# Kernel optimization log

Hardware: AMD Instinct MI355X
Metric: run time of the kernel (lower is better)

The kernel has to match this reference:

```python
import jax, jax.numpy as jnp
import numpy as np

N, H, V = 4096, 1024, 16384


def setup_inputs() -> dict:
    key = jax.random.key(0)
    k1, k2, k3, k4 = jax.random.split(key, 4)
    _input = jax.random.normal(k1, (N, H), dtype=jnp.float32)
    weight = jax.random.normal(k2, (V, H), dtype=jnp.float32) * (1.0 / np.sqrt(H))
    target = jax.random.normal(k3, (N, V), dtype=jnp.float32)
    bias = jax.random.normal(k4, (V,), dtype=jnp.float32)
    return {"_input": _input, "weight": weight, "target": target, "bias": bias}


def reference(_input, weight, target, bias):
    # Fused linear + MSE with reduction='mean':
    # logits = _input @ weight.T + bias  -> (N, V)
    # loss = mean((logits - target)**2) over all N*V elements
    logits = jnp.einsum("nh,vh->nv", _input, weight) + bias
    diff = logits - target
    return jnp.mean(diff * diff)
```

## Files before the change

### kernel.cpp

```cpp
#include <hip/hip_runtime.h>
#include <hip/hip_bf16.h>
#include <stdint.h>

#define N_ 4096
#define H_ 1024
#define V_ 16384

using i32x8  = __attribute__((ext_vector_type(8))) int;
using f32x16 = __attribute__((ext_vector_type(16))) float;

__global__ void cast2_f32_to_fp8(const float* __restrict__ in0, uint8_t* __restrict__ out0,
                                 const float* __restrict__ in1, uint8_t* __restrict__ out1,
                                 int nblk0) {
    const float* in;
    uint8_t* out;
    int bid;
    if (blockIdx.x < (unsigned)nblk0) { in = in0; out = out0; bid = blockIdx.x; }
    else                              { in = in1; out = out1; bid = blockIdx.x - nblk0; }
    size_t i = ((size_t)bid * blockDim.x + threadIdx.x) * 8;
    float4 a = *(const float4*)(in + i);
    float4 b = *(const float4*)(in + i + 4);
    int lo = __builtin_amdgcn_cvt_pk_fp8_f32(a.x, a.y, 0, 0);
    lo     = __builtin_amdgcn_cvt_pk_fp8_f32(a.z, a.w, lo, 1);
    int hi = __builtin_amdgcn_cvt_pk_fp8_f32(b.x, b.y, 0, 0);
    hi     = __builtin_amdgcn_cvt_pk_fp8_f32(b.z, b.w, hi, 1);
    *(int2*)(out + i) = make_int2(lo, hi);
}

#define BM 128
#define BN 128
#define BK 128

__global__ __launch_bounds__(256, 2) void gemm_mse(
    const uint8_t* __restrict__ A8,
    const uint8_t* __restrict__ W8,
    const float*  __restrict__ target,
    const float*  __restrict__ bias,
    float* __restrict__ partials)
{
    __shared__ uint8_t As[2 * 8 * 1024];
    __shared__ uint8_t Bs[2 * 8 * 1024];
    __shared__ float red[4];

    const int tid  = threadIdx.x;
    const int w    = tid >> 6;
    const int lane = tid & 63;
    const int l32  = lane & 31;
    const int half = lane >> 5;
    const int wm   = w >> 1;
    const int wn   = w & 1;

    const int flat = blockIdx.x;
    const int xcd  = flat & 7;
    const int idx  = flat >> 3;
    const int tx   = xcd * 16 + (idx & 15);
    const int ty   = idx >> 4;

    const int rowBase = ty * BM;
    const int colBase = tx * BN;

    f32x16 acc[2][2];
#pragma unroll
    for (int i = 0; i < 2; ++i)
#pragma unroll
        for (int j = 0; j < 2; ++j)
#pragma unroll
            for (int r = 0; r < 16; ++r) acc[i][j][r] = 0.f;

    const int ldrow = lane >> 2;
    const int ldkq  = (lane & 3) ^ ((ldrow + (ldrow >> 2)) & 3);

    const int rl  = lane & 15;
    const int rcb = (lane >> 4) & 1;
    const int fl  = (rl + (rl >> 2)) & 3;
    const uint8_t* aPtr[2][2];
    const uint8_t* bPtr[2][2];
#pragma unroll
    for (int i = 0; i < 2; ++i)
#pragma unroll
        for (int c = 0; c < 2; ++c) {
            const int slot = rl * 4 + (((half << 1) + c) ^ fl);
            aPtr[i][c] = As + (size_t)((wm * 2 + i) * 2 + rcb) * 1024 + slot * 16;
            bPtr[i][c] = Bs + (size_t)((wn * 2 + i) * 2 + rcb) * 1024 + slot * 16;
        }

    for (int k0 = 0; k0 < H_; k0 += BK) {
        __syncthreads();
#pragma unroll
        for (int h = 0; h < 2; ++h) {
#pragma unroll
            for (int c = 0; c < 2; ++c) {
                const int chunkid = w * 2 + c;
                const int kOff = k0 + h * 64 + ldkq * 16;
                const uint8_t* ga = A8 + (size_t)(rowBase + chunkid * 16 + ldrow) * H_ + kOff;
                __builtin_amdgcn_global_load_lds(
                    (const __attribute__((address_space(1))) void*)ga,
                    (__attribute__((address_space(3))) void*)(As + h * 8192 + chunkid * 1024), 16, 0, 0);
                const uint8_t* gb = W8 + (size_t)(colBase + chunkid * 16 + ldrow) * H_ + kOff;
                __builtin_amdgcn_global_load_lds(
                    (const __attribute__((address_space(1))) void*)gb,
                    (__attribute__((address_space(3))) void*)(Bs + h * 8192 + chunkid * 1024), 16, 0, 0);
            }
        }
        __syncthreads();

#pragma unroll
        for (int h = 0; h < 2; ++h) {
            i32x8 af[2], bq[2];
#pragma unroll
            for (int i = 0; i < 2; ++i) {
                int4 a0 = *(const int4*)(aPtr[i][0] + h * 8192);
                int4 a1 = *(const int4*)(aPtr[i][1] + h * 8192);
                af[i][0] = a0.x; af[i][1] = a0.y; af[i][2] = a0.z; af[i][3] = a0.w;
                af[i][4] = a1.x; af[i][5] = a1.y; af[i][6] = a1.z; af[i][7] = a1.w;
                int4 b0 = *(const int4*)(bPtr[i][0] + h * 8192);
                int4 b1 = *(const int4*)(bPtr[i][1] + h * 8192);
                bq[i][0] = b0.x; bq[i][1] = b0.y; bq[i][2] = b0.z; bq[i][3] = b0.w;
                bq[i][4] = b1.x; bq[i][5] = b1.y; bq[i][6] = b1.z; bq[i][7] = b1.w;
            }
#pragma unroll
            for (int i = 0; i < 2; ++i)
#pragma unroll
                for (int j = 0; j < 2; ++j)
                    acc[i][j] = __builtin_amdgcn_mfma_scale_f32_32x32x64_f8f6f4(
                        af[i], bq[j], acc[i][j],
                        0 , 0 ,
                        0, 0x7F7F7F7F,
                        0, 0x7F7F7F7F);
        }
    }

    float sum = 0.f;
    float biasj[2];
#pragma unroll
    for (int j = 0; j < 2; ++j) biasj[j] = bias[colBase + wn * 64 + j * 32 + l32];

#pragma unroll
    for (int i = 0; i < 2; ++i) {
#pragma unroll
        for (int r = 0; r < 16; ++r) {
            const int row = (r & 3) + 8 * (r >> 2) + 4 * half;
            const int gm = rowBase + wm * 64 + i * 32 + row;
            const float* trow = target + (size_t)gm * V_ + colBase + wn * 64 + l32;
#pragma unroll
            for (int j = 0; j < 2; ++j) {
                float d = acc[i][j][r] + biasj[j] - trow[j * 32];
                sum += d * d;
            }
        }
    }

#pragma unroll
    for (int off = 32; off; off >>= 1) sum += __shfl_down(sum, off, 64);
    if (lane == 0) red[w] = sum;
    __syncthreads();
    if (tid == 0)
        partials[flat] = red[0] + red[1] + red[2] + red[3];
}

__global__ void finalize_kernel(const float* __restrict__ partials, float* __restrict__ out, int n) {
    float s = 0.f;
    for (int i = threadIdx.x; i < n; i += 256) s += partials[i];
#pragma unroll
    for (int off = 32; off; off >>= 1) s += __shfl_down(s, off, 64);
    __shared__ float red[4];
    const int w = threadIdx.x >> 6, lane = threadIdx.x & 63;
    if (lane == 0) red[w] = s;
    __syncthreads();
    if (threadIdx.x == 0)
        out[0] = (red[0] + red[1] + red[2] + red[3]) * (1.0f / ((float)N_ * (float)V_));
}

extern "C" void kernel_launch(void* const* d_in, const int* in_sizes, int n_in,
                              void* d_out, int out_size, void* d_ws, size_t ws_size,
                              hipStream_t stream) {
    const float* input  = (const float*)d_in[0];
    const float* weight = (const float*)d_in[1];
    const float* target = (const float*)d_in[2];
    const float* bias   = (const float*)d_in[3];
    float* out = (float*)d_out;

    uint8_t* A8 = (uint8_t*)d_ws;
    uint8_t* W8 = A8 + (size_t)N_ * H_;
    float* partials = (float*)(W8 + (size_t)V_ * H_);

    const int nblk0 = (N_ * H_) / (256 * 8);
    const int nblk1 = (V_ * H_) / (256 * 8);
    cast2_f32_to_fp8<<<nblk0 + nblk1, 256, 0, stream>>>(input, A8, weight, W8, nblk0);

    const int nblocks = (V_ / BN) * (N_ / BM);
    gemm_mse<<<nblocks, 256, 0, stream>>>(A8, W8, target, bias, partials);

    finalize_kernel<<<1, 256, 0, stream>>>(partials, out, nblocks);
}
```

Before: 452.2 us.

## Enlarge GEMM tile to 256x256 with double-buffered LDS prefetch pipeline

Doubles the block tile to 256x256 with 512 threads (8 waves, each computing 128x64) to raise operand reuse per LDS byte and halve global fp8 reloads. Adds a 128KB dynamic-LDS double buffer so the next K-slice is loaded with global_load_lds while MFMAs run on the current one, replacing the two per-iteration __syncthreads with a single waitcnt+barrier. Raises wave priority around the MFMA block. The large LDS footprint limits occupancy to one block per CU and increases register pressure from the doubled accumulators.

```diff
diff --git a/kernel.cpp b/kernel.cpp
--- a/kernel.cpp
+++ b/kernel.cpp
@@ -27,41 +27,42 @@
     *(int2*)(out + i) = make_int2(lo, hi);
 }
 
-#define BM 128
-#define BN 128
+#define BM 256
+#define BN 256
 #define BK 128
 
-__global__ __launch_bounds__(256, 2) void gemm_mse(
+__global__ __launch_bounds__(512, 2) void gemm_mse(
     const uint8_t* __restrict__ A8,
     const uint8_t* __restrict__ W8,
     const float*  __restrict__ target,
     const float*  __restrict__ bias,
     float* __restrict__ partials)
 {
-    __shared__ uint8_t As[2 * 8 * 1024];
-    __shared__ uint8_t Bs[2 * 8 * 1024];
-    __shared__ float red[4];
+    extern __shared__ __align__(16) uint8_t smem[];
+    uint8_t* As = smem;
+    uint8_t* Bs = smem + 65536;
+    __shared__ float red[8];
 
     const int tid  = threadIdx.x;
     const int w    = tid >> 6;
     const int lane = tid & 63;
     const int l32  = lane & 31;
     const int half = lane >> 5;
-    const int wm   = w >> 1;
-    const int wn   = w & 1;
+    const int wm   = w >> 2;
+    const int wn   = w & 3;
 
     const int flat = blockIdx.x;
     const int xcd  = flat & 7;
     const int idx  = flat >> 3;
-    const int tx   = xcd * 16 + (idx & 15);
-    const int ty   = idx >> 4;
+    const int tx   = xcd * 8 + (idx & 7);
+    const int ty   = idx >> 3;
 
     const int rowBase = ty * BM;
     const int colBase = tx * BN;
 
-    f32x16 acc[2][2];
-#pragma unroll
-    for (int i = 0; i < 2; ++i)
+    f32x16 acc[4][2];
+#pragma unroll
+    for (int i = 0; i < 4; ++i)
 #pragma unroll
         for (int j = 0; j < 2; ++j)
 #pragma unroll
@@ -73,53 +74,74 @@
     const int rl  = lane & 15;
     const int rcb = (lane >> 4) & 1;
     const int fl  = (rl + (rl >> 2)) & 3;
-    const uint8_t* aPtr[2][2];
-    const uint8_t* bPtr[2][2];
-#pragma unroll
-    for (int i = 0; i < 2; ++i)
+    int aOff[4][2], bOff[2][2];
+#pragma unroll
+    for (int i = 0; i < 4; ++i)
 #pragma unroll
         for (int c = 0; c < 2; ++c) {
             const int slot = rl * 4 + (((half << 1) + c) ^ fl);
-            aPtr[i][c] = As + (size_t)((wm * 2 + i) * 2 + rcb) * 1024 + slot * 16;
-            bPtr[i][c] = Bs + (size_t)((wn * 2 + i) * 2 + rcb) * 1024 + slot * 16;
-        }
-
-    for (int k0 = 0; k0 < H_; k0 += BK) {
-        __syncthreads();
+            aOff[i][c] = (wm * 8 + i * 2 + rcb) * 1024 + slot * 16;
+        }
+#pragma unroll
+    for (int j = 0; j < 2; ++j)
+#pragma unroll
+        for (int c = 0; c < 2; ++c) {
+            const int slot = rl * 4 + (((half << 1) + c) ^ fl);
+            bOff[j][c] = (wn * 4 + j * 2 + rcb) * 1024 + slot * 16;
+        }
+
+    auto STAGE = [&](int t, int buf) {
+        const int kT = t * BK;
 #pragma unroll
         for (int h = 0; h < 2; ++h) {
 #pragma unroll
             for (int c = 0; c < 2; ++c) {
-                const int chunkid = w * 2 + c;
-                const int kOff = k0 + h * 64 + ldkq * 16;
-                const uint8_t* ga = A8 + (size_t)(rowBase + chunkid * 16 + ldrow) * H_ + kOff;
+                const int cid  = w * 2 + c;
+                const int kOff = kT + h * 64 + ldkq * 16;
+                const uint8_t* ga = A8 + (size_t)(rowBase + cid * 16 + ldrow) * H_ + kOff;
                 __builtin_amdgcn_global_load_lds(
                     (const __attribute__((address_space(1))) void*)ga,
-                    (__attribute__((address_space(3))) void*)(As + h * 8192 + chunkid * 1024), 16, 0, 0);
-                const uint8_t* gb = W8 + (size_t)(colBase + chunkid * 16 + ldrow) * H_ + kOff;
+                    (__attribute__((address_space(3))) void*)(As + buf * 32768 + h * 16384 + cid * 1024),
+                    16, 0, 0);
+                const uint8_t* gb = W8 + (size_t)(colBase + cid * 16 + ldrow) * H_ + kOff;
                 __builtin_amdgcn_global_load_lds(
                     (const __attribute__((address_space(1))) void*)gb,
-                    (__attribute__((address_space(3))) void*)(Bs + h * 8192 + chunkid * 1024), 16, 0, 0);
-            }
-        }
-        __syncthreads();
-
+                    (__attribute__((address_space(3))) void*)(Bs + buf * 32768 + h * 16384 + cid * 1024),
+                    16, 0, 0);
+            }
+        }
+    };
+
+    STAGE(0, 0);
+    asm volatile("s_waitcnt vmcnt(0)" ::: "memory");
+    __builtin_amdgcn_s_barrier();
+    asm volatile("" ::: "memory");
+
+    int cur = 0;
+    for (int t = 0; t < 8; ++t) {
+        if (t < 7) STAGE(t + 1, cur ^ 1);
+        const uint8_t* aB = As + cur * 32768;
+        const uint8_t* bB = Bs + cur * 32768;
 #pragma unroll
         for (int h = 0; h < 2; ++h) {
-            i32x8 af[2], bq[2];
-#pragma unroll
-            for (int i = 0; i < 2; ++i) {
-                int4 a0 = *(const int4*)(aPtr[i][0] + h * 8192);
-                int4 a1 = *(const int4*)(aPtr[i][1] + h * 8192);
+            i32x8 af[4], bq[2];
+#pragma unroll
+            for (int i = 0; i < 4; ++i) {
+                int4 a0 = *(const int4*)(aB + h * 16384 + aOff[i][0]);
+                int4 a1 = *(const int4*)(aB + h * 16384 + aOff[i][1]);
                 af[i][0] = a0.x; af[i][1] = a0.y; af[i][2] = a0.z; af[i][3] = a0.w;
                 af[i][4] = a1.x; af[i][5] = a1.y; af[i][6] = a1.z; af[i][7] = a1.w;
-                int4 b0 = *(const int4*)(bPtr[i][0] + h * 8192);
-                int4 b1 = *(const int4*)(bPtr[i][1] + h * 8192);
-                bq[i][0] = b0.x; bq[i][1] = b0.y; bq[i][2] = b0.z; bq[i][3] = b0.w;
-                bq[i][4] = b1.x; bq[i][5] = b1.y; bq[i][6] = b1.z; bq[i][7] = b1.w;
-            }
-#pragma unroll
-            for (int i = 0; i < 2; ++i)
+            }
+#pragma unroll
+            for (int j = 0; j < 2; ++j) {
+                int4 b0 = *(const int4*)(bB + h * 16384 + bOff[j][0]);
+                int4 b1 = *(const int4*)(bB + h * 16384 + bOff[j][1]);
+                bq[j][0] = b0.x; bq[j][1] = b0.y; bq[j][2] = b0.z; bq[j][3] = b0.w;
+                bq[j][4] = b1.x; bq[j][5] = b1.y; bq[j][6] = b1.z; bq[j][7] = b1.w;
+            }
+            __builtin_amdgcn_s_setprio(1);
+#pragma unroll
+            for (int i = 0; i < 4; ++i)
 #pragma unroll
                 for (int j = 0; j < 2; ++j)
                     acc[i][j] = __builtin_amdgcn_mfma_scale_f32_32x32x64_f8f6f4(
@@ -127,7 +149,13 @@
                         0 , 0 ,
                         0, 0x7F7F7F7F,
                         0, 0x7F7F7F7F);
-        }
+            __builtin_amdgcn_s_setprio(0);
+        }
+        if (t < 7) asm volatile("s_waitcnt vmcnt(0)" ::: "memory");
+        asm volatile("" ::: "memory");
+        __builtin_amdgcn_s_barrier();
+        asm volatile("" ::: "memory");
+        cur ^= 1;
     }
 
     float sum = 0.f;
@@ -136,11 +164,11 @@
     for (int j = 0; j < 2; ++j) biasj[j] = bias[colBase + wn * 64 + j * 32 + l32];
 
 #pragma unroll
-    for (int i = 0; i < 2; ++i) {
+    for (int i = 0; i < 4; ++i) {
 #pragma unroll
         for (int r = 0; r < 16; ++r) {
             const int row = (r & 3) + 8 * (r >> 2) + 4 * half;
-            const int gm = rowBase + wm * 64 + i * 32 + row;
+            const int gm = rowBase + wm * 128 + i * 32 + row;
             const float* trow = target + (size_t)gm * V_ + colBase + wn * 64 + l32;
 #pragma unroll
             for (int j = 0; j < 2; ++j) {
@@ -154,8 +182,12 @@
     for (int off = 32; off; off >>= 1) sum += __shfl_down(sum, off, 64);
     if (lane == 0) red[w] = sum;
     __syncthreads();
-    if (tid == 0)
-        partials[flat] = red[0] + red[1] + red[2] + red[3];
+    if (tid == 0) {
+        float s = 0.f;
+#pragma unroll
+        for (int i = 0; i < 8; ++i) s += red[i];
+        partials[flat] = s;
+    }
 }
 
 __global__ void finalize_kernel(const float* __restrict__ partials, float* __restrict__ out, int n) {
@@ -189,7 +221,7 @@
     cast2_f32_to_fp8<<<nblk0 + nblk1, 256, 0, stream>>>(input, A8, weight, W8, nblk0);
 
     const int nblocks = (V_ / BN) * (N_ / BM);
-    gemm_mse<<<nblocks, 256, 0, stream>>>(A8, W8, target, bias, partials);
+    gemm_mse<<<nblocks, 512, 131072, stream>>>(A8, W8, target, bias, partials);
 
     finalize_kernel<<<1, 256, 0, stream>>>(partials, out, nblocks);
 }
```

Result: slower. 465.7 us (+3.0%).

## Double-buffer LDS K-tiles and prefetch target values during GEMM tail

Applied to the files above, without the earlier changes.

Switches the fp8 GEMM main loop to double-buffered dynamic shared memory (64 KB), issuing the next K tile's global-to-LDS loads before computing the current one, with one barrier per iteration instead of two. Target tile values are loaded into registers during the last two K iterations so the MSE epilogue latency overlaps the MFMA work. s_setprio is raised around the MFMA block. The trade-off is double the LDS footprint, which at 256 threads may limit occupancy to 2 blocks/CU on 160 KB LDS, plus 64 extra registers for prefetched targets.

```diff
diff --git a/kernel.cpp b/kernel.cpp
--- a/kernel.cpp
+++ b/kernel.cpp
@@ -38,8 +38,9 @@
     const float*  __restrict__ bias,
     float* __restrict__ partials)
 {
-    __shared__ uint8_t As[2 * 8 * 1024];
-    __shared__ uint8_t Bs[2 * 8 * 1024];
+    extern __shared__ __align__(16) uint8_t smem[];
+    uint8_t* As = smem;
+    uint8_t* Bs = smem + 32768;
     __shared__ float red[4];
 
     const int tid  = threadIdx.x;
@@ -73,51 +74,91 @@
     const int rl  = lane & 15;
     const int rcb = (lane >> 4) & 1;
     const int fl  = (rl + (rl >> 2)) & 3;
-    const uint8_t* aPtr[2][2];
-    const uint8_t* bPtr[2][2];
+    int aOff[2][2], bOff[2][2];
 #pragma unroll
     for (int i = 0; i < 2; ++i)
 #pragma unroll
         for (int c = 0; c < 2; ++c) {
             const int slot = rl * 4 + (((half << 1) + c) ^ fl);
-            aPtr[i][c] = As + (size_t)((wm * 2 + i) * 2 + rcb) * 1024 + slot * 16;
-            bPtr[i][c] = Bs + (size_t)((wn * 2 + i) * 2 + rcb) * 1024 + slot * 16;
-        }
-
-    for (int k0 = 0; k0 < H_; k0 += BK) {
-        __syncthreads();
+            aOff[i][c] = ((wm * 2 + i) * 2 + rcb) * 1024 + slot * 16;
+            bOff[i][c] = ((wn * 2 + i) * 2 + rcb) * 1024 + slot * 16;
+        }
+
+    float biasj[2];
+#pragma unroll
+    for (int j = 0; j < 2; ++j) biasj[j] = bias[colBase + wn * 64 + j * 32 + l32];
+
+    auto STAGE = [&](int t, int buf) {
+        const int kT = t * BK;
 #pragma unroll
         for (int h = 0; h < 2; ++h) {
 #pragma unroll
             for (int c = 0; c < 2; ++c) {
-                const int chunkid = w * 2 + c;
-                const int kOff = k0 + h * 64 + ldkq * 16;
-                const uint8_t* ga = A8 + (size_t)(rowBase + chunkid * 16 + ldrow) * H_ + kOff;
+                const int cid  = w * 2 + c;
+                const int kOff = kT + h * 64 + ldkq * 16;
+                const uint8_t* ga = A8 + (size_t)(rowBase + cid * 16 + ldrow) * H_ + kOff;
                 __builtin_amdgcn_global_load_lds(
                     (const __attribute__((address_space(1))) void*)ga,
-                    (__attribute__((address_space(3))) void*)(As + h * 8192 + chunkid * 1024), 16, 0, 0);
-                const uint8_t* gb = W8 + (size_t)(colBase + chunkid * 16 + ldrow) * H_ + kOff;
+                    (__attribute__((address_space(3))) void*)(As + buf * 16384 + h * 8192 + cid * 1024),
+                    16, 0, 0);
+                const uint8_t* gb = W8 + (size_t)(colBase + cid * 16 + ldrow) * H_ + kOff;
                 __builtin_amdgcn_global_load_lds(
                     (const __attribute__((address_space(1))) void*)gb,
-                    (__attribute__((address_space(3))) void*)(Bs + h * 8192 + chunkid * 1024), 16, 0, 0);
-            }
-        }
-        __syncthreads();
-
+                    (__attribute__((address_space(3))) void*)(Bs + buf * 16384 + h * 8192 + cid * 1024),
+                    16, 0, 0);
+            }
+        }
+    };
+
+    float tgt0[16][2], tgt1[16][2];
+
+    STAGE(0, 0);
+    asm volatile("s_waitcnt vmcnt(0)" ::: "memory");
+    __builtin_amdgcn_s_barrier();
+    asm volatile("" ::: "memory");
+
+    int cur = 0;
+    for (int t = 0; t < 8; ++t) {
+        if (t < 7) STAGE(t + 1, cur ^ 1);
+        asm volatile("" ::: "memory");
+        if (t == 6) {
+#pragma unroll
+            for (int r = 0; r < 16; ++r) {
+                const int row = (r & 3) + 8 * (r >> 2) + 4 * half;
+                const float* trow = target + (size_t)(rowBase + wm * 64 + 0 * 32 + row) * V_
+                                    + colBase + wn * 64 + l32;
+                tgt0[r][0] = trow[0];
+                tgt0[r][1] = trow[32];
+            }
+        }
+        if (t == 7) {
+#pragma unroll
+            for (int r = 0; r < 16; ++r) {
+                const int row = (r & 3) + 8 * (r >> 2) + 4 * half;
+                const float* trow = target + (size_t)(rowBase + wm * 64 + 1 * 32 + row) * V_
+                                    + colBase + wn * 64 + l32;
+                tgt1[r][0] = trow[0];
+                tgt1[r][1] = trow[32];
+            }
+        }
+
+        const uint8_t* aB = As + cur * 16384;
+        const uint8_t* bB = Bs + cur * 16384;
 #pragma unroll
         for (int h = 0; h < 2; ++h) {
             i32x8 af[2], bq[2];
 #pragma unroll
             for (int i = 0; i < 2; ++i) {
-                int4 a0 = *(const int4*)(aPtr[i][0] + h * 8192);
-                int4 a1 = *(const int4*)(aPtr[i][1] + h * 8192);
+                int4 a0 = *(const int4*)(aB + h * 8192 + aOff[i][0]);
+                int4 a1 = *(const int4*)(aB + h * 8192 + aOff[i][1]);
                 af[i][0] = a0.x; af[i][1] = a0.y; af[i][2] = a0.z; af[i][3] = a0.w;
                 af[i][4] = a1.x; af[i][5] = a1.y; af[i][6] = a1.z; af[i][7] = a1.w;
-                int4 b0 = *(const int4*)(bPtr[i][0] + h * 8192);
-                int4 b1 = *(const int4*)(bPtr[i][1] + h * 8192);
+                int4 b0 = *(const int4*)(bB + h * 8192 + bOff[i][0]);
+                int4 b1 = *(const int4*)(bB + h * 8192 + bOff[i][1]);
                 bq[i][0] = b0.x; bq[i][1] = b0.y; bq[i][2] = b0.z; bq[i][3] = b0.w;
                 bq[i][4] = b1.x; bq[i][5] = b1.y; bq[i][6] = b1.z; bq[i][7] = b1.w;
             }
+            __builtin_amdgcn_s_setprio(1);
 #pragma unroll
             for (int i = 0; i < 2; ++i)
 #pragma unroll
@@ -127,26 +168,32 @@
                         0 , 0 ,
                         0, 0x7F7F7F7F,
                         0, 0x7F7F7F7F);
-        }
+            __builtin_amdgcn_s_setprio(0);
+        }
+
+        if (t < 7) {
+            asm volatile("s_waitcnt vmcnt(0)" ::: "memory");
+            __builtin_amdgcn_s_barrier();
+            asm volatile("" ::: "memory");
+        }
+        cur ^= 1;
     }
 
     float sum = 0.f;
-    float biasj[2];
-#pragma unroll
-    for (int j = 0; j < 2; ++j) biasj[j] = bias[colBase + wn * 64 + j * 32 + l32];
-
-#pragma unroll
-    for (int i = 0; i < 2; ++i) {
-#pragma unroll
-        for (int r = 0; r < 16; ++r) {
-            const int row = (r & 3) + 8 * (r >> 2) + 4 * half;
-            const int gm = rowBase + wm * 64 + i * 32 + row;
-            const float* trow = target + (size_t)gm * V_ + colBase + wn * 64 + l32;
-#pragma unroll
-            for (int j = 0; j < 2; ++j) {
-                float d = acc[i][j][r] + biasj[j] - trow[j * 32];
-                sum += d * d;
-            }
+#pragma unroll
+    for (int r = 0; r < 16; ++r) {
+#pragma unroll
+        for (int j = 0; j < 2; ++j) {
+            float d = acc[0][j][r] + biasj[j] - tgt0[r][j];
+            sum += d * d;
+        }
+    }
+#pragma unroll
+    for (int r = 0; r < 16; ++r) {
+#pragma unroll
+        for (int j = 0; j < 2; ++j) {
+            float d = acc[1][j][r] + biasj[j] - tgt1[r][j];
+            sum += d * d;
         }
     }
 
@@ -189,7 +236,7 @@
     cast2_f32_to_fp8<<<nblk0 + nblk1, 256, 0, stream>>>(input, A8, weight, W8, nblk0);
 
     const int nblocks = (V_ / BN) * (N_ / BM);
-    gemm_mse<<<nblocks, 256, 0, stream>>>(A8, W8, target, bias, partials);
+    gemm_mse<<<nblocks, 256, 65536, stream>>>(A8, W8, target, bias, partials);
 
     finalize_kernel<<<1, 256, 0, stream>>>(partials, out, nblocks);
 }
```

Measured after the change: 455.4 us. No clear change (+0.7%).

## Double-buffer LDS K-tiles with prefetch overlapping MFMA compute

Applied to the files above, without the earlier changes.

The K tile shrinks from 128 to 64 and the loop becomes a two-stage LDS ping-pong. The next tile's global-to-LDS loads are issued before the current tile's MFMAs, with one barrier per iteration instead of two. This is meant to hide global load latency behind matrix math rather than stalling on every tile. Launch bounds rise to 4 blocks per CU for more occupancy, and s_setprio boosts priority around the MFMA block. The trade-offs are more loop iterations and barriers overall, and possible register pressure from the tighter occupancy bound.

```diff
diff --git a/kernel.cpp b/kernel.cpp
--- a/kernel.cpp
+++ b/kernel.cpp
@@ -29,17 +29,17 @@
 
 #define BM 128
 #define BN 128
-#define BK 128
-
-__global__ __launch_bounds__(256, 2) void gemm_mse(
+#define BK 64
+
+__global__ __launch_bounds__(256, 4) void gemm_mse(
     const uint8_t* __restrict__ A8,
     const uint8_t* __restrict__ W8,
     const float*  __restrict__ target,
     const float*  __restrict__ bias,
     float* __restrict__ partials)
 {
-    __shared__ uint8_t As[2 * 8 * 1024];
-    __shared__ uint8_t Bs[2 * 8 * 1024];
+    __shared__ __align__(16) uint8_t As[2][8192];
+    __shared__ __align__(16) uint8_t Bs[2][8192];
     __shared__ float red[4];
 
     const int tid  = threadIdx.x;
@@ -73,68 +73,84 @@
     const int rl  = lane & 15;
     const int rcb = (lane >> 4) & 1;
     const int fl  = (rl + (rl >> 2)) & 3;
-    const uint8_t* aPtr[2][2];
-    const uint8_t* bPtr[2][2];
+    int aOff[2][2], bOff[2][2];
 #pragma unroll
     for (int i = 0; i < 2; ++i)
 #pragma unroll
         for (int c = 0; c < 2; ++c) {
             const int slot = rl * 4 + (((half << 1) + c) ^ fl);
-            aPtr[i][c] = As + (size_t)((wm * 2 + i) * 2 + rcb) * 1024 + slot * 16;
-            bPtr[i][c] = Bs + (size_t)((wn * 2 + i) * 2 + rcb) * 1024 + slot * 16;
-        }
-
-    for (int k0 = 0; k0 < H_; k0 += BK) {
-        __syncthreads();
-#pragma unroll
-        for (int h = 0; h < 2; ++h) {
-#pragma unroll
-            for (int c = 0; c < 2; ++c) {
-                const int chunkid = w * 2 + c;
-                const int kOff = k0 + h * 64 + ldkq * 16;
-                const uint8_t* ga = A8 + (size_t)(rowBase + chunkid * 16 + ldrow) * H_ + kOff;
-                __builtin_amdgcn_global_load_lds(
-                    (const __attribute__((address_space(1))) void*)ga,
-                    (__attribute__((address_space(3))) void*)(As + h * 8192 + chunkid * 1024), 16, 0, 0);
-                const uint8_t* gb = W8 + (size_t)(colBase + chunkid * 16 + ldrow) * H_ + kOff;
-                __builtin_amdgcn_global_load_lds(
-                    (const __attribute__((address_space(1))) void*)gb,
-                    (__attribute__((address_space(3))) void*)(Bs + h * 8192 + chunkid * 1024), 16, 0, 0);
-            }
-        }
-        __syncthreads();
-
-#pragma unroll
-        for (int h = 0; h < 2; ++h) {
-            i32x8 af[2], bq[2];
-#pragma unroll
-            for (int i = 0; i < 2; ++i) {
-                int4 a0 = *(const int4*)(aPtr[i][0] + h * 8192);
-                int4 a1 = *(const int4*)(aPtr[i][1] + h * 8192);
-                af[i][0] = a0.x; af[i][1] = a0.y; af[i][2] = a0.z; af[i][3] = a0.w;
-                af[i][4] = a1.x; af[i][5] = a1.y; af[i][6] = a1.z; af[i][7] = a1.w;
-                int4 b0 = *(const int4*)(bPtr[i][0] + h * 8192);
-                int4 b1 = *(const int4*)(bPtr[i][1] + h * 8192);
-                bq[i][0] = b0.x; bq[i][1] = b0.y; bq[i][2] = b0.z; bq[i][3] = b0.w;
-                bq[i][4] = b1.x; bq[i][5] = b1.y; bq[i][6] = b1.z; bq[i][7] = b1.w;
-            }
-#pragma unroll
-            for (int i = 0; i < 2; ++i)
-#pragma unroll
-                for (int j = 0; j < 2; ++j)
-                    acc[i][j] = __builtin_amdgcn_mfma_scale_f32_32x32x64_f8f6f4(
-                        af[i], bq[j], acc[i][j],
-                        0 , 0 ,
-                        0, 0x7F7F7F7F,
-                        0, 0x7F7F7F7F);
-        }
+            aOff[i][c] = ((wm * 2 + i) * 2 + rcb) * 1024 + slot * 16;
+            bOff[i][c] = ((wn * 2 + i) * 2 + rcb) * 1024 + slot * 16;
+        }
+
+    float biasj[2];
+#pragma unroll
+    for (int j = 0; j < 2; ++j) biasj[j] = bias[colBase + wn * 64 + j * 32 + l32];
+
+    auto STAGE = [&](int t, int buf) {
+        const int kT = t * BK;
+#pragma unroll
+        for (int c = 0; c < 2; ++c) {
+            const int cid  = w * 2 + c;
+            const int kOff = kT + ldkq * 16;
+            const uint8_t* ga = A8 + (size_t)(rowBase + cid * 16 + ldrow) * H_ + kOff;
+            __builtin_amdgcn_global_load_lds(
+                (const __attribute__((address_space(1))) void*)ga,
+                (__attribute__((address_space(3))) void*)(&As[buf][0] + cid * 1024),
+                16, 0, 0);
+            const uint8_t* gb = W8 + (size_t)(colBase + cid * 16 + ldrow) * H_ + kOff;
+            __builtin_amdgcn_global_load_lds(
+                (const __attribute__((address_space(1))) void*)gb,
+                (__attribute__((address_space(3))) void*)(&Bs[buf][0] + cid * 1024),
+                16, 0, 0);
+        }
+    };
+
+    STAGE(0, 0);
+    asm volatile("s_waitcnt vmcnt(0)" ::: "memory");
+    __builtin_amdgcn_s_barrier();
+    asm volatile("" ::: "memory");
+
+    int cur = 0;
+    for (int t = 0; t < 16; ++t) {
+        if (t < 15) STAGE(t + 1, cur ^ 1);
+        asm volatile("" ::: "memory");
+
+        const uint8_t* aB = &As[cur][0];
+        const uint8_t* bB = &Bs[cur][0];
+        i32x8 af[2], bq[2];
+#pragma unroll
+        for (int i = 0; i < 2; ++i) {
+            int4 a0 = *(const int4*)(aB + aOff[i][0]);
+            int4 a1 = *(const int4*)(aB + aOff[i][1]);
+            af[i][0] = a0.x; af[i][1] = a0.y; af[i][2] = a0.z; af[i][3] = a0.w;
+            af[i][4] = a1.x; af[i][5] = a1.y; af[i][6] = a1.z; af[i][7] = a1.w;
+            int4 b0 = *(const int4*)(bB + bOff[i][0]);
+            int4 b1 = *(const int4*)(bB + bOff[i][1]);
+            bq[i][0] = b0.x; bq[i][1] = b0.y; bq[i][2] = b0.z; bq[i][3] = b0.w;
+            bq[i][4] = b1.x; bq[i][5] = b1.y; bq[i][6] = b1.z; bq[i][7] = b1.w;
+        }
+        __builtin_amdgcn_s_setprio(1);
+#pragma unroll
+        for (int i = 0; i < 2; ++i)
+#pragma unroll
+            for (int j = 0; j < 2; ++j)
+                acc[i][j] = __builtin_amdgcn_mfma_scale_f32_32x32x64_f8f6f4(
+                    af[i], bq[j], acc[i][j],
+                    0 , 0 ,
+                    0, 0x7F7F7F7F,
+                    0, 0x7F7F7F7F);
+        __builtin_amdgcn_s_setprio(0);
+
+        if (t < 15) {
+            asm volatile("s_waitcnt vmcnt(0)" ::: "memory");
+            __builtin_amdgcn_s_barrier();
+            asm volatile("" ::: "memory");
+        }
+        cur ^= 1;
     }
 
     float sum = 0.f;
-    float biasj[2];
-#pragma unroll
-    for (int j = 0; j < 2; ++j) biasj[j] = bias[colBase + wn * 64 + j * 32 + l32];
-
 #pragma unroll
     for (int i = 0; i < 2; ++i) {
 #pragma unroll
```

After: 455.7 us. Within noise of the previous version (+0.8%).
